# Kernel tuning notes

Hardware: AMD Instinct MI355X
Metric: run time of the kernel (lower is better)

The kernel has to match this reference:

```python
import jax, jax.numpy as jnp
import numpy as np

V = 30000   # vocab (from get_word_embedding default)
D = 640     # d_model
L = 6       # num_layers
H = 8       # num_heads
DH = D // H # head dim 80
FF = 4 * D  # ffn hidden 2560
BOS = 1
EOS = 2
LN_EPS = 1e-6


def _ln(x, s, b):
    m = x.mean(-1, keepdims=True)
    v = ((x - m) ** 2).mean(-1, keepdims=True)
    return (x - m) / jnp.sqrt(v + LN_EPS) * s + b


def _get_logits(tokens, seq_len, emb, Wq, bq, Wk, bk, Wv, bv, Wo, bo,
                ln1s, ln1b, W1, b1, W2, b2, ln2s, ln2b, lmW, lmb):
    # tokens: (B,S) int; seq_len: (B,) int
    B, S = tokens.shape
    h = emb[tokens]                                   # (B,S,D), no pos-enc / scaling in source
    look_ahead = jnp.triu(jnp.ones((S, S), jnp.float32), k=1)          # 1 = masked (TF-style)
    pad = (jnp.arange(S)[None, :] >= seq_len[:, None]).astype(jnp.float32)  # (B,S)
    mask = jnp.maximum(look_ahead[None, None, :, :], pad[:, None, None, :])  # (B,1,S,S)

    def layer(h, p):
        wq, bq_, wk, bk_, wv, bv_, wo, bo_, l1s, l1b, w1, b1_, w2, b2_, l2s, l2b = p
        q = (h @ wq + bq_).reshape(B, S, H, DH)
        k = (h @ wk + bk_).reshape(B, S, H, DH)
        v = (h @ wv + bv_).reshape(B, S, H, DH)
        scores = jnp.einsum('bqhd,bkhd->bhqk', q, k) / jnp.sqrt(jnp.float32(DH))
        scores = scores - mask * 1e9
        a = jax.nn.softmax(scores, axis=-1)
        o = jnp.einsum('bhqk,bkhd->bqhd', a, v).reshape(B, S, D) @ wo + bo_
        h = _ln(h + o, l1s, l1b)                      # post-LN residual
        f = jax.nn.relu(h @ w1 + b1_) @ w2 + b2_
        h = _ln(h + f, l2s, l2b)
        return h, None

    h, _ = jax.lax.scan(layer, h, (Wq, bq, Wk, bk, Wv, bv, Wo, bo,
                                   ln1s, ln1b, W1, b1, W2, b2, ln2s, ln2b))
    return h @ lmW + lmb                              # (B,S,V)


def setup_inputs() -> dict:
    key = jax.random.key(0)
    ks = jax.random.split(key, 12)
    std = 0.02

    def n(k, shape):
        return jax.random.normal(k, shape, jnp.float32) * std

    return {
        'initial_words': jax.random.randint(ks[0], (4, 8), 3, V, dtype=jnp.int32),
        'max_length': 32,
        'emb': n(ks[1], (V, D)),
        'Wq': n(ks[2], (L, D, D)), 'bq': jnp.zeros((L, D), jnp.float32),
        'Wk': n(ks[3], (L, D, D)), 'bk': jnp.zeros((L, D), jnp.float32),
        'Wv': n(ks[4], (L, D, D)), 'bv': jnp.zeros((L, D), jnp.float32),
        'Wo': n(ks[5], (L, D, D)), 'bo': jnp.zeros((L, D), jnp.float32),
        'ln1s': jnp.ones((L, D), jnp.float32), 'ln1b': jnp.zeros((L, D), jnp.float32),
        'W1': n(ks[6], (L, D, FF)), 'b1': jnp.zeros((L, FF), jnp.float32),
        'W2': n(ks[7], (L, FF, D)), 'b2': jnp.zeros((L, D), jnp.float32),
        'ln2s': jnp.ones((L, D), jnp.float32), 'ln2b': jnp.zeros((L, D), jnp.float32),
        'lmW': n(ks[8], (D, V)), 'lmb': jnp.zeros((V,), jnp.float32),
    }


def reference(initial_words, max_length, emb, Wq, bq, Wk, bk, Wv, bv, Wo, bo,
              ln1s, ln1b, W1, b1, W2, b2, ln2s, ln2b, lmW, lmb):
    B, init_len = initial_words.shape
    seq_len = jnp.full((B,), max_length, jnp.int32)
    S = max_length + 1  # BOS + max_length slots, as in the torch padding logic
    inp = (jnp.zeros((B, S), jnp.int32)
           .at[:, 0].set(BOS)
           .at[:, 1:1 + init_len].set(initial_words.astype(jnp.int32)))

    def cond(c):
        _inp, cl, tok = c
        return (cl + 1 <= max_length) & jnp.any(tok != EOS)

    def body(c):
        inp, cl, _tok = c
        logits = _get_logits(inp, seq_len, emb, Wq, bq, Wk, bk, Wv, bv, Wo, bo,
                             ln1s, ln1b, W1, b1, W2, b2, ln2s, ln2b, lmW, lmb)
        step_logits = jax.lax.dynamic_index_in_dim(logits, cl, axis=1, keepdims=False)
        tok = jnp.argmax(step_logits, axis=-1).astype(jnp.int32)
        inp = inp.at[:, cl + 1].set(tok)
        return (inp, cl + 1, tok)

    inp, _, _ = jax.lax.while_loop(
        cond, body,
        (inp, jnp.int32(init_len), jnp.full((B,), -100, jnp.int32)))
    return inp[:, 1:]
```

## Files before the change

kernel.cpp:

```cpp
#include <hip/hip_runtime.h>
#include <math.h>

#define B 4
#define SEQ 33
#define MAXLEN 32
#define D 640
#define NH 8
#define DH 80
#define NL 6
#define FF 2560
#define V 30000
#define INITLEN 8
#define NBLK 1024
#define NT 256
#define EOS_TOK 2
#define NPOS_P 9
#define NR_P 36
#define LM_NB 938

#define QKV_N 120
#define AW_B 120
#define RF_B 184
#define F1_B 188
#define F2_B 348
#define RL_B 428

#define NFLAGS 1024
#define NSLOT 32
#define SLOT_U 16

#define VER(t,l) ((size_t)((t) * NL + (l)))

typedef float f4 __attribute__((ext_vector_type(4)));

struct Par {
  const int* iw;
  const float* emb;
  const float *Wq, *bq, *Wk, *bk, *Wv, *bv, *Wo, *bo;
  const float *ln1s, *ln1b, *W1, *b1, *W2, *b2, *ln2s, *ln2b, *lmW, *lmb;
  int* out;
};

__device__ __align__(256) float g_Kc[(size_t)NL * B * NH * SEQ * DH];
__device__ __align__(256) float g_Vc[(size_t)NL * B * NH * SEQ * DH];
__device__ __align__(256) float g_xv[(size_t)SEQ * NL * 2560];
__device__ __align__(256) float g_h1v[(size_t)SEQ * NL * 2560];
__device__ __align__(256) float g_qv[(size_t)SEQ * NL * 2560];
__device__ __align__(256) float g_opartv[(size_t)SEQ * NL * 20480];
__device__ __align__(256) float g_f1v[(size_t)SEQ * NL * 10240];
__device__ __align__(256) float g_f2v[(size_t)SEQ * NL * 5120];
__device__ __align__(256) float g_xlm[(size_t)SEQ * 2560];
__device__ __align__(256) int   g_tokv[SEQ * 64];
__device__ __align__(256) int   g_stopv[SEQ * 64];
__device__ float g_xp[NR_P * D];
__device__ float g_h1p[NR_P * D];
__device__ float g_qkvpP[(size_t)8 * 1920 * NR_P];
__device__ float g_qP[(size_t)NH * NR_P * DH];
__device__ float g_opartP[(size_t)NH * D * NR_P];
__device__ float g_f1pP[(size_t)8 * FF * NR_P];
__device__ float g_f2pP[(size_t)32 * D * NR_P];
__device__ unsigned long long g_keys[(size_t)NBLK * B];
__device__ int g_tokens[B * SEQ];
__device__ unsigned g_flags[(size_t)NFLAGS * NSLOT * SLOT_U];
__device__ unsigned g_arrive = 0;
__device__ unsigned g_gen = 0;

#define KCIDX(l,b,h,pos,j) (((((size_t)(l)*B+(b))*NH+(h))*SEQ+(pos))*DH+(j))

__device__ __forceinline__ float ldc(const float* p) {
  return __hip_atomic_load(p, __ATOMIC_RELAXED, __HIP_MEMORY_SCOPE_AGENT);
}
__device__ __forceinline__ void stc(float* p, float v) {
  __hip_atomic_store(p, v, __ATOMIC_RELAXED, __HIP_MEMORY_SCOPE_AGENT);
}
__device__ __forceinline__ int ldci(const int* p) {
  return __hip_atomic_load(p, __ATOMIC_RELAXED, __HIP_MEMORY_SCOPE_AGENT);
}
__device__ __forceinline__ void stci(int* p, int v) {
  __hip_atomic_store(p, v, __ATOMIC_RELAXED, __HIP_MEMORY_SCOPE_AGENT);
}
__device__ __forceinline__ void stcu64(unsigned long long* p, unsigned long long v) {
  __hip_atomic_store(p, v, __ATOMIC_RELAXED, __HIP_MEMORY_SCOPE_AGENT);
}
__device__ __forceinline__ void st4c(float* p, f4 v) {
  asm volatile("global_store_dwordx4 %0, %1, off sc1" :: "v"(p), "v"(v) : "memory");
}
__device__ __forceinline__ void ld4c_issue(f4& dst, const float* p) {
  asm volatile("global_load_dwordx4 %0, %1, off sc1" : "=v"(dst) : "v"(p) : "memory");
}
__device__ __forceinline__ void wait_vm() {
  asm volatile("s_waitcnt vmcnt(0)" ::: "memory");
  __builtin_amdgcn_sched_barrier(0);
}
__device__ __forceinline__ unsigned long long mk64(float lo, float hi) {
  return ((unsigned long long)__float_as_uint(hi) << 32) | (unsigned long long)__float_as_uint(lo);
}

__device__ __forceinline__ void gsync_full() {
  __syncthreads();
  if (threadIdx.x == 0) {
    __threadfence();
    unsigned g = __hip_atomic_load(&g_gen, __ATOMIC_SEQ_CST, __HIP_MEMORY_SCOPE_AGENT);
    unsigned old = __hip_atomic_fetch_add(&g_arrive, 1u, __ATOMIC_SEQ_CST, __HIP_MEMORY_SCOPE_AGENT);
    if (old == NBLK - 1u) {
      __hip_atomic_store(&g_arrive, 0u, __ATOMIC_SEQ_CST, __HIP_MEMORY_SCOPE_AGENT);
      __hip_atomic_fetch_add(&g_gen, 1u, __ATOMIC_SEQ_CST, __HIP_MEMORY_SCOPE_AGENT);
    } else {
      while (__hip_atomic_load(&g_gen, __ATOMIC_RELAXED, __HIP_MEMORY_SCOPE_AGENT) == g)
        __builtin_amdgcn_s_sleep(2);
    }
    __threadfence();
  }
  __syncthreads();
}

__device__ __forceinline__ void stage_done(int idx) {
  asm volatile("s_waitcnt vmcnt(0)" ::: "memory");
  __syncthreads();
  if (threadIdx.x == 0) {
    __hip_atomic_fetch_add(
        &g_flags[((size_t)idx * NSLOT + (blockIdx.x & (NSLOT - 1))) * SLOT_U],
        1u, __ATOMIC_RELAXED, __HIP_MEMORY_SCOPE_AGENT);
  }
}

__device__ __forceinline__ void stage_wait(int idx, unsigned cnt) {
  if (threadIdx.x < 64) {
    const unsigned* base = &g_flags[(size_t)idx * NSLOT * SLOT_U];
    int spins = 0;
    for (;;) {
      unsigned v = 0u;
      if (threadIdx.x < NSLOT)
        v = __hip_atomic_load(base + (size_t)threadIdx.x * SLOT_U,
                              __ATOMIC_RELAXED, __HIP_MEMORY_SCOPE_AGENT);
      #pragma unroll
      for (int o = 16; o > 0; o >>= 1) v += __shfl_down(v, o, 64);
      v = __shfl(v, 0, 64);
      if (v >= cnt) break;
      if (spins < 16)      __builtin_amdgcn_s_sleep(1);
      else if (spins < 96) __builtin_amdgcn_s_sleep(16);
      else                 __builtin_amdgcn_s_sleep(127);
      ++spins;
    }
  }
  __syncthreads();
  asm volatile("" ::: "memory");
}

__device__ __forceinline__ float bred_sum(float v, float* s_red) {
  #pragma unroll
  for (int o = 32; o > 0; o >>= 1) v += __shfl_down(v, o, 64);
  __syncthreads();
  if ((threadIdx.x & 63) == 0) s_red[threadIdx.x >> 6] = v;
  __syncthreads();
  return s_red[0] + s_red[1] + s_red[2] + s_red[3];
}

__device__ void ln_inplace(float* row, const float* gam, const float* bet, float* s_red) {
  float ps = 0.f;
  for (int d = threadIdx.x; d < D; d += NT) ps += row[d];
  const float m = bred_sum(ps, s_red) * (1.0f / 640.0f);
  float pv = 0.f;
  for (int d = threadIdx.x; d < D; d += NT) { float t = row[d] - m; pv += t * t; }
  const float var = bred_sum(pv, s_red) * (1.0f / 640.0f);
  const float rstd = 1.0f / sqrtf(var + 1e-6f);
  for (int d = threadIdx.x; d < D; d += NT)
    row[d] = (row[d] - m) * rstd * gam[d] + bet[d];
  __syncthreads();
}


__device__ void st_QKV(const Par& p, int l, int t, float* s_x, float* s_t, float* s_r) {
  const int tid = threadIdx.x;
  const int cg = (blockIdx.x & 7) * 15 + (blockIdx.x >> 3);
  const int m = cg / 40, colm0 = (cg % 40) * 16;
  const int w = tid >> 6, lane = tid & 63;
  if (l == 0) {
    const int tok = g_tokv[t * 64 + w];
    for (int c4 = lane; c4 < 160; c4 += 64)
      *(f4*)&s_x[w * 640 + c4 * 4] = *(const f4*)&p.emb[(size_t)tok * D + c4 * 4];
  } else {
    const size_t ver = VER(t, l - 1);
    const float* h1 = g_h1v + ver * 2560 + w * 640;
    const float* fa = g_f2v + ver * 5120 + w * 640;
    const float* fb = g_f2v + ver * 5120 + 2560 + w * 640;
    const float* b2 = p.b2 + (size_t)(l - 1) * D;
    for (int c4 = lane; c4 < 160; c4 += 64) {
      f4 a = *(const f4*)&h1[c4 * 4];
      f4 b = *(const f4*)&fa[c4 * 4];
      f4 c = *(const f4*)&fb[c4 * 4];
      const float* bb = b2 + c4 * 4;
      f4 s = { a.x + b.x + c.x + bb[0], a.y + b.y + c.y + bb[1],
               a.z + b.z + c.z + bb[2], a.w + b.w + c.w + bb[3] };
      *(f4*)&s_x[w * 640 + c4 * 4] = s;
    }
    float ps = 0.f;
    for (int i = lane; i < D; i += 64) ps += s_x[w * 640 + i];
    #pragma unroll
    for (int o = 32; o > 0; o >>= 1) ps += __shfl_xor(ps, o, 64);
    const float mean = ps * (1.0f / 640.0f);
    float pv = 0.f;
    for (int i = lane; i < D; i += 64) { float d = s_x[w * 640 + i] - mean; pv += d * d; }
    #pragma unroll
    for (int o = 32; o > 0; o >>= 1) pv += __shfl_xor(pv, o, 64);
    const float rstd = 1.0f / sqrtf(pv * (1.0f / 640.0f) + 1e-6f);
    const float* gam = p.ln2s + (size_t)(l - 1) * D;
    const float* bet = p.ln2b + (size_t)(l - 1) * D;
    for (int i = lane; i < D; i += 64)
      s_x[w * 640 + i] = (s_x[w * 640 + i] - mean) * rstd * gam[i] + bet[i];
  }
  __syncthreads();
  if (cg == 0) {
    const size_t xo = VER(t, l) * 2560;
    for (int i = tid; i < 640; i += NT)
      st4c(&g_xv[xo + (size_t)i * 4], *(f4*)&s_x[i * 4]);
  }
  const int ds = tid >> 4, c = tid & 15;
  const float* Wb = (m == 0 ? p.Wq : m == 1 ? p.Wk : p.Wv)
                    + (size_t)l * D * D + colm0 + c;
  float a0 = 0, a1 = 0, a2 = 0, a3 = 0;
  #pragma unroll
  for (int kb = 0; kb < 40; kb += 20) {
    float wv[20];
    #pragma unroll
    for (int j = 0; j < 20; ++j) wv[j] = Wb[(size_t)(ds + (kb + j) * 16) * D];
    #pragma unroll
    for (int j = 0; j < 20; ++j) {
      const int dd = ds + (kb + j) * 16;
      a0 = fmaf(s_x[dd],        wv[j], a0);
      a1 = fmaf(s_x[640 + dd],  wv[j], a1);
      a2 = fmaf(s_x[1280 + dd], wv[j], a2);
      a3 = fmaf(s_x[1920 + dd], wv[j], a3);
    }
  }
  { f4 av = { a0, a1, a2, a3 }; *(f4*)&s_t[c * 68 + ds * 4] = av; }
  __syncthreads();
  if (tid < 64) {
    const int c2 = tid >> 2, b = tid & 3;
    float v = 0.f;
    #pragma unroll
    for (int d2 = 0; d2 < 16; ++d2) v += s_t[c2 * 68 + d2 * 4 + b];
    v += (m == 0 ? p.bq : m == 1 ? p.bk : p.bv)[(size_t)l * D + colm0 + c2];
    s_r[c2 * 4 + b] = v;
  }
  __syncthreads();
  if (m == 0) {
    if (tid < 16) {
      f4 v = { s_r[tid * 4], s_r[tid * 4 + 1], s_r[tid * 4 + 2], s_r[tid * 4 + 3] };
      st4c(&g_qv[VER(t, l) * 2560 + (size_t)(colm0 + tid) * 4], v);
    }
  } else {
    const int h = colm0 / 80, j0 = colm0 % 80;
    if (tid < 16) {
      const int cq = tid & 3, b = tid >> 2;
      f4 v = { s_r[(cq*4+0)*4+b], s_r[(cq*4+1)*4+b], s_r[(cq*4+2)*4+b], s_r[(cq*4+3)*4+b] };
      float* cache = (m == 1) ? g_Kc : g_Vc;
      st4c(&cache[KCIDX(l, b, h, t, j0 + cq * 4)], v);
    }
  }
}

__device__ void st_AW(const Par& p, int l, int t,
                      float* s_q, float* s_sc, float* s_o, float* s_wo) {
  const int idx = blockIdx.x - AW_B, h = idx >> 3, c = idx & 7, tid = threadIdx.x;
  const size_t qo = VER(t, l) * 2560;
  if (tid < 80) {
    f4 q = *(const f4*)&g_qv[qo + (size_t)(h * 80 + tid) * 4];
    s_q[tid] = q.x; s_q[80 + tid] = q.y; s_q[160 + tid] = q.z; s_q[240 + tid] = q.w;
  }
  __syncthreads();
  const int nk = t + 1;
  for (int task = tid; task < 4 * nk; task += NT) {
    const int b = task / nk, kp = task % nk;
    const float* qq = s_q + b * 80;
    const f4* kk = (const f4*)&g_Kc[KCIDX(l, b, h, kp, 0)];
    float sd = 0.f;
    #pragma unroll
    for (int j4 = 0; j4 < 20; ++j4) {
      f4 k4 = kk[j4];
      sd += qq[j4*4+0]*k4.x + qq[j4*4+1]*k4.y + qq[j4*4+2]*k4.z + qq[j4*4+3]*k4.w;
    }
    s_sc[b * 33 + kp] = sd / 8.94427190999915878564f;
  }
  __syncthreads();
  if (tid < 4) {
    const int b = tid;
    float m = -1e30f;
    for (int k = 0; k < nk; ++k) m = fmaxf(m, s_sc[b * 33 + k]);
    float sum = 0.f;
    for (int k = 0; k < nk; ++k) { float e = expf(s_sc[b * 33 + k] - m); s_sc[b * 33 + k] = e; sum += e; }
    s_sc[132 + b] = 1.0f / sum;
  }
  __syncthreads();
  if (tid < 80) {
    const int b = tid / 20, j4 = tid % 20;
    f4 acc = { 0.f, 0.f, 0.f, 0.f };
    for (int kp = 0; kp < nk; ++kp) {
      f4 v = *(const f4*)&g_Vc[KCIDX(l, b, h, kp, j4 * 4)];
      const float wgt = s_sc[b * 33 + kp];
      acc.x += wgt * v.x; acc.y += wgt * v.y; acc.z += wgt * v.z; acc.w += wgt * v.w;
    }
    const float r = s_sc[132 + b];
    f4 o = { acc.x * r, acc.y * r, acc.z * r, acc.w * r };
    *(f4*)&s_o[b * 80 + j4 * 4] = o;
  }
  __syncthreads();
  if (tid < 240) {
    const int j = tid % 80, sub = tid / 80;
    const int col = c * 80 + j;
    const int d0 = sub * 27, d1 = (sub == 2) ? 80 : d0 + 27;
    const float* Wo = p.Wo + (size_t)l * D * D + col;
    float a0 = 0, a1 = 0, a2 = 0, a3 = 0;
    #pragma unroll 9
    for (int dd = d0; dd < d1; ++dd) {
      const float w = Wo[(size_t)(h * 80 + dd) * D];
      a0 += s_o[0*80+dd] * w; a1 += s_o[80+dd] * w;
      a2 += s_o[160+dd] * w; a3 += s_o[240+dd] * w;
    }
    float* tp = s_wo + (j * 3 + sub) * 4;
    tp[0] = a0; tp[1] = a1; tp[2] = a2; tp[3] = a3;
  }
  __syncthreads();
  if (tid < 80) {
    const int b = tid / 20, cq = tid % 20;
    f4 v;
    #pragma unroll
    for (int i = 0; i < 4; ++i) {
      const int j = cq * 4 + i;
      v[i] = s_wo[(j*3+0)*4+b] + s_wo[(j*3+1)*4+b] + s_wo[(j*3+2)*4+b];
    }
    st4c(&g_opartv[VER(t, l) * 20480 + (size_t)(h * 4 + b) * 640 + c * 80 + cq * 4], v);
  }
}

__device__ void st_RF(const Par& p, int l, int t, float* s_row, float* s_red) {
  const int b = blockIdx.x - RF_B, tid = threadIdx.x;
  const size_t ver = VER(t, l);
  if (tid < 160) {
    f4 xv = *(const f4*)&g_xv[ver * 2560 + (size_t)b * 640 + tid * 4];
    const float* bo = p.bo + (size_t)l * D + tid * 4;
    f4 a;
    a.x = xv.x + bo[0]; a.y = xv.y + bo[1]; a.z = xv.z + bo[2]; a.w = xv.w + bo[3];
    #pragma unroll
    for (int h = 0; h < 8; ++h) {
      f4 ov = *(const f4*)&g_opartv[ver * 20480 + (size_t)(h * 4 + b) * 640 + tid * 4];
      a.x += ov.x; a.y += ov.y; a.z += ov.z; a.w += ov.w;
    }
    *(f4*)&s_row[tid * 4] = a;
  }
  __syncthreads();
  ln_inplace(s_row, p.ln1s + (size_t)l * D, p.ln1b + (size_t)l * D, s_red);
  if (tid < 160) st4c(&g_h1v[ver * 2560 + (size_t)b * 640 + tid * 4], *(f4*)&s_row[tid * 4]);
}

__device__ void st_F1(const Par& p, int l, int t, float* s_x, float* s_t, float* s_r) {
  const int tid = threadIdx.x;
  const int raw = blockIdx.x - F1_B;
  const int cg = (raw & 7) * 20 + (raw >> 3);
  const int col0 = cg * 16;
  const size_t ver = VER(t, l);
  #pragma unroll
  for (int i = 0; i < 3; ++i) {
    const int idx = tid + i * NT;
    if (idx < 640) *(f4*)&s_x[idx * 4] = *(const f4*)&g_h1v[ver * 2560 + (size_t)idx * 4];
  }
  __syncthreads();
  const int ds = tid >> 4, c = tid & 15;
  const float* Wb = p.W1 + (size_t)l * D * FF + col0 + c;
  float a0 = 0, a1 = 0, a2 = 0, a3 = 0;
  #pragma unroll
  for (int kb = 0; kb < 40; kb += 20) {
    float wv[20];
    #pragma unroll
    for (int j = 0; j < 20; ++j) wv[j] = Wb[(size_t)(ds + (kb + j) * 16) * FF];
    #pragma unroll
    for (int j = 0; j < 20; ++j) {
      const int dd = ds + (kb + j) * 16;
      a0 = fmaf(s_x[dd],        wv[j], a0);
      a1 = fmaf(s_x[640 + dd],  wv[j], a1);
      a2 = fmaf(s_x[1280 + dd], wv[j], a2);
      a3 = fmaf(s_x[1920 + dd], wv[j], a3);
    }
  }
  { f4 av = { a0, a1, a2, a3 }; *(f4*)&s_t[c * 68 + ds * 4] = av; }
  __syncthreads();
  if (tid < 64) {
    const int c2 = tid >> 2, b = tid & 3;
    float v = 0.f;
    #pragma unroll
    for (int d2 = 0; d2 < 16; ++d2) v += s_t[c2 * 68 + d2 * 4 + b];
    v += p.b1[(size_t)l * FF + col0 + c2];
    s_r[c2 * 4 + b] = fmaxf(v, 0.f);
  }
  __syncthreads();
  if (tid < 16) {
    const int cq = tid & 3, b = tid >> 2;
    f4 v = { s_r[(cq*4+0)*4+b], s_r[(cq*4+1)*4+b], s_r[(cq*4+2)*4+b], s_r[(cq*4+3)*4+b] };
    st4c(&g_f1v[ver * 10240 + (size_t)b * 2560 + col0 + cq * 4], v);
  }
}

__device__ void st_F2(const Par& p, int l, int t, float* s_f, float* s_t, float* s_r) {
  const int idx = blockIdx.x - F2_B, tid = threadIdx.x;
  const int hf = idx / 40, craw = idx % 40;
  const int cg = (craw & 7) * 5 + (craw >> 3);
  const int col0 = cg * 16;
  const size_t ver = VER(t, l);
  #pragma unroll
  for (int i = 0; i < 5; ++i) {
    const int ii = tid + i * NT;
    const int b = ii / 320, fo = ii % 320;
    *(f4*)&s_f[b * 1280 + fo * 4] =
        *(const f4*)&g_f1v[ver * 10240 + (size_t)b * 2560 + hf * 1280 + fo * 4];
  }
  __syncthreads();
  const int ds = tid >> 4, c = tid & 15;
  const float* Wb = p.W2 + (size_t)l * FF * D + (size_t)hf * 1280 * D + col0 + c;
  float a0 = 0, a1 = 0, a2 = 0, a3 = 0;
  #pragma unroll
  for (int kb = 0; kb < 80; kb += 20) {
    float wv[20];
    #pragma unroll
    for (int j = 0; j < 20; ++j) wv[j] = Wb[(size_t)(ds + (kb + j) * 16) * D];
    #pragma unroll
    for (int j = 0; j < 20; ++j) {
      const int dl = ds + (kb + j) * 16;
      a0 = fmaf(s_f[dl],        wv[j], a0);
      a1 = fmaf(s_f[1280 + dl], wv[j], a1);
      a2 = fmaf(s_f[2560 + dl], wv[j], a2);
      a3 = fmaf(s_f[3840 + dl], wv[j], a3);
    }
  }
  { f4 av = { a0, a1, a2, a3 }; *(f4*)&s_t[c * 68 + ds * 4] = av; }
  __syncthreads();
  if (tid < 64) {
    const int c2 = tid >> 2, b = tid & 3;
    float v = 0.f;
    #pragma unroll
    for (int d2 = 0; d2 < 16; ++d2) v += s_t[c2 * 68 + d2 * 4 + b];
    s_r[c2 * 4 + b] = v;
  }
  __syncthreads();
  if (tid < 16) {
    const int cq = tid & 3, b = tid >> 2;
    f4 v = { s_r[(cq*4+0)*4+b], s_r[(cq*4+1)*4+b], s_r[(cq*4+2)*4+b], s_r[(cq*4+3)*4+b] };
    st4c(&g_f2v[ver * 5120 + (size_t)(hf * 4 + b) * 640 + col0 + cq * 4], v);
  }
}

__device__ void st_RL(const Par& p, int t, float* s_row, float* s_red) {
  const int b = blockIdx.x - RL_B, tid = threadIdx.x;
  const size_t ver = VER(t, NL - 1);
  if (tid < 160) {
    f4 h  = *(const f4*)&g_h1v[ver * 2560 + (size_t)b * 640 + tid * 4];
    f4 fa = *(const f4*)&g_f2v[ver * 5120 + (size_t)b * 640 + tid * 4];
    f4 fb = *(const f4*)&g_f2v[ver * 5120 + 2560 + (size_t)b * 640 + tid * 4];
    const float* b2 = p.b2 + (size_t)(NL - 1) * D + tid * 4;
    f4 a;
    a.x = h.x + fa.x + fb.x + b2[0];
    a.y = h.y + fa.y + fb.y + b2[1];
    a.z = h.z + fa.z + fb.z + b2[2];
    a.w = h.w + fa.w + fb.w + b2[3];
    *(f4*)&s_row[tid * 4] = a;
  }
  __syncthreads();
  ln_inplace(s_row, p.ln2s + (size_t)(NL - 1) * D, p.ln2b + (size_t)(NL - 1) * D, s_red);
  if (tid < 160)
    st4c(&g_xlm[(size_t)t * 2560 + (size_t)b * 640 + tid * 4], *(f4*)&s_row[tid * 4]);
}

__device__ void st_LM(const Par& p, int t, float* s_xf, float* s_part, unsigned long long* s_key) {
  const int bid = blockIdx.x, tid = threadIdx.x;
  const int xcd = bid & 7, jj = bid >> 3;
  const int chunk = (xcd < 2 ? xcd * 118 : 236 + (xcd - 2) * 117) + jj;
  #pragma unroll
  for (int i = 0; i < 3; ++i) {
    const int idx = tid + i * NT;
    if (idx < 640) *(f4*)&s_xf[idx * 4] = *(const f4*)&g_xlm[(size_t)t * 2560 + (size_t)idx * 4];
  }
  __syncthreads();
  const int sg = tid >> 5, cj = tid & 31;
  const int col = chunk * 32 + cj;
  float a0 = 0, a1 = 0, a2 = 0, a3 = 0;
  if (col < V) {
    const float* W = p.lmW + (size_t)sg * 80 * V + col;
    #pragma unroll
    for (int kb = 0; kb < 80; kb += 20) {
      float w[20];
      #pragma unroll
      for (int j = 0; j < 20; ++j) w[j] = W[(size_t)(kb + j) * V];
      #pragma unroll
      for (int j = 0; j < 20; ++j) {
        const int d = sg * 80 + kb + j;
        a0 = fmaf(s_xf[d],        w[j], a0);
        a1 = fmaf(s_xf[640 + d],  w[j], a1);
        a2 = fmaf(s_xf[1280 + d], w[j], a2);
        a3 = fmaf(s_xf[1920 + d], w[j], a3);
      }
    }
  }
  float* tp = s_part + (sg * 32 + cj) * 4;
  tp[0] = a0; tp[1] = a1; tp[2] = a2; tp[3] = a3;
  __syncthreads();
  if (tid < 128) {
    const int cj2 = tid >> 2, b = tid & 3, col2 = chunk * 32 + cj2;
    unsigned long long key = 0ull;
    if (col2 < V) {
      float a = p.lmb[col2];
      #pragma unroll
      for (int sg2 = 0; sg2 < 8; ++sg2) a += s_part[(sg2 * 32 + cj2) * 4 + b];
      unsigned u = __float_as_uint(a);
      u = (u & 0x80000000u) ? ~u : (u | 0x80000000u);
      key = ((unsigned long long)u << 32) | (unsigned)(V - col2);
    }
    s_key[cj2 * 4 + b] = key;
  }
  __syncthreads();
  if (tid < 4) {
    unsigned long long k0 = 0ull;
    for (int cj2 = 0; cj2 < 32; ++cj2) {
      const unsigned long long k = s_key[cj2 * 4 + tid];
      if (k > k0) k0 = k;
    }
    stcu64(&g_keys[(size_t)bid * B + tid], k0);
  }
}

__device__ void st_CTL(int t, unsigned long long* s_k64, int* s_ctl) {
  const int tid = threadIdx.x;
  const int i0 = tid, i1 = tid + NT, i2 = tid + 2 * NT, i3 = tid + 3 * NT;
  f4 z = { 0.f, 0.f, 0.f, 0.f };
  f4 ka0, kb0, ka1, kb1, ka2, kb2, ka3 = z, kb3 = z;
  ld4c_issue(ka0, (const float*)&g_keys[(size_t)i0 * 4]);
  ld4c_issue(kb0, (const float*)&g_keys[(size_t)i0 * 4 + 2]);
  ld4c_issue(ka1, (const float*)&g_keys[(size_t)i1 * 4]);
  ld4c_issue(kb1, (const float*)&g_keys[(size_t)i1 * 4 + 2]);
  ld4c_issue(ka2, (const float*)&g_keys[(size_t)i2 * 4]);
  ld4c_issue(kb2, (const float*)&g_keys[(size_t)i2 * 4 + 2]);
  if (i3 < LM_NB) {
    ld4c_issue(ka3, (const float*)&g_keys[(size_t)i3 * 4]);
    ld4c_issue(kb3, (const float*)&g_keys[(size_t)i3 * 4 + 2]);
  }
  wait_vm();
  unsigned long long m0 = mk64(ka0.x, ka0.y), m1 = mk64(ka0.z, ka0.w);
  unsigned long long m2 = mk64(kb0.x, kb0.y), m3 = mk64(kb0.z, kb0.w);
  { unsigned long long s;
    s = mk64(ka1.x,ka1.y); if (s>m0) m0=s;  s = mk64(ka1.z,ka1.w); if (s>m1) m1=s;
    s = mk64(kb1.x,kb1.y); if (s>m2) m2=s;  s = mk64(kb1.z,kb1.w); if (s>m3) m3=s;
    s = mk64(ka2.x,ka2.y); if (s>m0) m0=s;  s = mk64(ka2.z,ka2.w); if (s>m1) m1=s;
    s = mk64(kb2.x,kb2.y); if (s>m2) m2=s;  s = mk64(kb2.z,kb2.w); if (s>m3) m3=s;
    s = mk64(ka3.x,ka3.y); if (s>m0) m0=s;  s = mk64(ka3.z,ka3.w); if (s>m1) m1=s;
    s = mk64(kb3.x,kb3.y); if (s>m2) m2=s;  s = mk64(kb3.z,kb3.w); if (s>m3) m3=s;
  }
  #pragma unroll
  for (int o = 32; o > 0; o >>= 1) {
    unsigned long long s;
    s = __shfl_down(m0, o, 64); if (s > m0) m0 = s;
    s = __shfl_down(m1, o, 64); if (s > m1) m1 = s;
    s = __shfl_down(m2, o, 64); if (s > m2) m2 = s;
    s = __shfl_down(m3, o, 64); if (s > m3) m3 = s;
  }
  if ((tid & 63) == 0) {
    const int w = tid >> 6;
    s_k64[w * 4 + 0] = m0; s_k64[w * 4 + 1] = m1;
    s_k64[w * 4 + 2] = m2; s_k64[w * 4 + 3] = m3;
  }
  __syncthreads();
  if (tid == 0) {
    #pragma unroll
    for (int b = 0; b < B; ++b) {
      unsigned long long k0 = s_k64[b];
      #pragma unroll
      for (int w = 1; w < 4; ++w) if (s_k64[w * 4 + b] > k0) k0 = s_k64[w * 4 + b];
      const int tok = V - (int)(unsigned)(k0 & 0xFFFFFFFFull);
      stci(&g_tokens[b * SEQ + t + 1], tok);
      stci(&g_tokv[(t + 1) * 64 + b], tok);
      s_ctl[b] = tok;
    }
    int stop = (t == MAXLEN - 1) ? 1 : 0;
    if (s_ctl[0] == EOS_TOK && s_ctl[1] == EOS_TOK &&
        s_ctl[2] == EOS_TOK && s_ctl[3] == EOS_TOK) stop = 1;
    stci(&g_stopv[t * 64], stop);
  }
}


__device__ void st_Qp(const Par& p, int l, float* s_a) {
  const int idx = blockIdx.x, tid = threadIdx.x;
  const int h = idx / 24, rem = idx % 24, s = rem / 3, rg = rem % 3;
  const int r0 = rg * 12, d0 = s * 80;
  for (int i = tid; i < 960; i += NT) {
    const int ri = i / 80, dd = i % 80;
    s_a[i] = ldc(&g_xp[(r0 + ri) * D + d0 + dd]);
  }
  __syncthreads();
  if (tid < 240) {
    const int m = tid / 80, j = tid % 80, col = h * 80 + j;
    const float* W = (m == 0 ? p.Wq : m == 1 ? p.Wk : p.Wv) + (size_t)l * D * D + col;
    float acc[12];
    #pragma unroll
    for (int ri = 0; ri < 12; ++ri) acc[ri] = 0.f;
    for (int dd = 0; dd < 80; ++dd) {
      const float w = W[(size_t)(d0 + dd) * D];
      #pragma unroll
      for (int ri = 0; ri < 12; ++ri) acc[ri] += s_a[ri * 80 + dd] * w;
    }
    float* o = g_qkvpP + ((size_t)s * 1920 + m * 640 + col) * NR_P + r0;
    #pragma unroll
    for (int ri = 0; ri < 12; ++ri) stc(o + ri, acc[ri]);
  }
}

__device__ void st_AWp1(const Par& p, int l) {
  const int idx = blockIdx.x - 192, h = idx >> 2, c = idx & 3, tid = threadIdx.x;
  for (int pp = c; pp < NPOS_P; pp += 4) {
    for (int task = tid; task < 960; task += NT) {
      const int m = task / 320, rem = task % 320, j = rem >> 2, b = rem & 3;
      const int r = pp * 4 + b;
      const int col = m * 640 + h * 80 + j;
      const float* q = g_qkvpP + (size_t)col * NR_P + r;
      float a = 0.f;
      #pragma unroll
      for (int s = 0; s < 8; ++s) a += ldc(q + (size_t)s * 1920 * NR_P);
      a += (m == 0 ? p.bq : m == 1 ? p.bk : p.bv)[(size_t)l * D + h * 80 + j];
      if (m == 0)      stc(&g_qP[((size_t)h * NR_P + r) * DH + j], a);
      else if (m == 1) stc(&g_Kc[KCIDX(l, b, h, pp, j)], a);
      else             stc(&g_Vc[KCIDX(l, b, h, pp, j)], a);
    }
  }
}

__device__ void st_AWp2(const Par& p, int l, float* s_a, float* s_b, float* s_c) {
  const int idx = blockIdx.x - 224, h = idx >> 2, rg = idx & 3, tid = threadIdx.x;
  const int r0 = rg * 9;
  for (int i = tid; i < 720; i += NT) {
    const int ri = i / 80, j = i % 80;
    s_a[i] = ldc(&g_qP[((size_t)h * NR_P + r0 + ri) * DH + j]);
  }
  __syncthreads();
  for (int task = tid; task < 81; task += NT) {
    const int ri = task / 9, kp = task % 9;
    const int r = r0 + ri, pos = r >> 2, b = r & 3;
    if (kp <= pos) {
      const float* kk = g_Kc + KCIDX(l, b, h, kp, 0);
      const float* qq = s_a + ri * 80;
      float sd = 0.f;
      for (int j = 0; j < 80; ++j) sd += qq[j] * ldc(kk + j);
      s_c[ri * 9 + kp] = sd / 8.94427190999915878564f;
    }
  }
  __syncthreads();
  if (tid < 9) {
    const int ri = tid, r = r0 + ri, pos = r >> 2;
    float m = -1e30f;
    for (int k = 0; k <= pos; ++k) m = fmaxf(m, s_c[ri * 9 + k]);
    float sum = 0.f;
    for (int k = 0; k <= pos; ++k) { float e = expf(s_c[ri * 9 + k] - m); s_c[ri * 9 + k] = e; sum += e; }
    s_c[81 + ri] = 1.0f / sum;
  }
  __syncthreads();
  for (int task = tid; task < 720; task += NT) {
    const int ri = task / 80, j = task % 80;
    const int r = r0 + ri, pos = r >> 2, b = r & 3;
    float acc = 0.f;
    for (int kp = 0; kp <= pos; ++kp)
      acc += s_c[ri * 9 + kp] * ldc(&g_Vc[KCIDX(l, b, h, kp, j)]);
    s_b[ri * 80 + j] = acc * s_c[81 + ri];
  }
  __syncthreads();
  if (tid < 160) {
    for (int pass = 0; pass < 4; ++pass) {
      const int col = pass * 160 + tid;
      const float* Wo = p.Wo + (size_t)l * D * D + col;
      float acc[9];
      #pragma unroll
      for (int ri = 0; ri < 9; ++ri) acc[ri] = 0.f;
      for (int dd = 0; dd < 80; ++dd) {
        const float w = Wo[(size_t)(h * 80 + dd) * D];
        #pragma unroll
        for (int ri = 0; ri < 9; ++ri) acc[ri] += s_b[ri * 80 + dd] * w;
      }
      #pragma unroll
      for (int ri = 0; ri < 9; ++ri)
        stc(&g_opartP[((size_t)h * D + col) * NR_P + r0 + ri], acc[ri]);
    }
  }
}

__device__ void st_RFp(const Par& p, int l, float* s_row, float* s_red) {
  const int r = blockIdx.x, tid = threadIdx.x;
  for (int col = tid; col < D; col += NT) {
    float a = ldc(&g_xp[r * D + col]) + p.bo[(size_t)l * D + col];
    #pragma unroll
    for (int h = 0; h < 8; ++h) a += ldc(&g_opartP[((size_t)h * D + col) * NR_P + r]);
    s_row[col] = a;
  }
  __syncthreads();
  ln_inplace(s_row, p.ln1s + (size_t)l * D, p.ln1b + (size_t)l * D, s_red);
  for (int col = tid; col < D; col += NT) stc(&g_h1p[r * D + col], s_row[col]);
}

__device__ void st_F1p(const Par& p, int l, float* s_a) {
  const int idx = blockIdx.x, tid = threadIdx.x;
  const int s = idx / 30, rem = idx % 30, cg = rem / 3, rg = rem % 3;
  const int r0 = rg * 12, d0 = s * 80;
  for (int i = tid; i < 960; i += NT) {
    const int ri = i / 80, dd = i % 80;
    s_a[i] = ldc(&g_h1p[(r0 + ri) * D + d0 + dd]);
  }
  __syncthreads();
  const int col = cg * 256 + tid;
  const float* W = p.W1 + (size_t)l * D * FF + col;
  float acc[12];
  #pragma unroll
  for (int ri = 0; ri < 12; ++ri) acc[ri] = 0.f;
  for (int dd = 0; dd < 80; ++dd) {
    const float w = W[(size_t)(d0 + dd) * FF];
    #pragma unroll
    for (int ri = 0; ri < 12; ++ri) acc[ri] += s_a[ri * 80 + dd] * w;
  }
  float* o = g_f1pP + ((size_t)s * FF + col) * NR_P + r0;
  #pragma unroll
  for (int ri = 0; ri < 12; ++ri) stc(o + ri, acc[ri]);
}

__device__ void st_F2p(const Par& p, int l, float* s_c) {
  const int idx = blockIdx.x - 240, c = idx / 3, rg = idx % 3, tid = threadIdx.x;
  const int r0 = rg * 12;
  for (int task = tid; task < 960; task += NT) {
    const int ri = task / 80, fj = task % 80;
    const int fcol = c * 80 + fj;
    const float* pp = g_f1pP + (size_t)fcol * NR_P + r0 + ri;
    float a = 0.f;
    #pragma unroll
    for (int s = 0; s < 8; ++s) a += ldc(pp + (size_t)s * FF * NR_P);
    a += p.b1[(size_t)l * FF + fcol];
    s_c[ri * 80 + fj] = fmaxf(a, 0.f);
  }
  __syncthreads();
  for (int pass = 0; pass < 3; ++pass) {
    const int col = pass * 256 + tid;
    if (col < D) {
      const float* W = p.W2 + (size_t)l * FF * D + col;
      float acc[12];
      #pragma unroll
      for (int ri = 0; ri < 12; ++ri) acc[ri] = 0.f;
      for (int fj = 0; fj < 80; ++fj) {
        const float w = W[(size_t)(c * 80 + fj) * D];
        #pragma unroll
        for (int ri = 0; ri < 12; ++ri) acc[ri] += s_c[ri * 80 + fj] * w;
      }
      float* o = g_f2pP + ((size_t)c * D + col) * NR_P + r0;
      #pragma unroll
      for (int ri = 0; ri < 12; ++ri) stc(o + ri, acc[ri]);
    }
  }
}

__device__ void st_RQp(const Par& p, int l, float* s_row, float* s_red) {
  const int r = blockIdx.x, tid = threadIdx.x;
  for (int col = tid; col < D; col += NT) {
    float a = ldc(&g_h1p[r * D + col]) + p.b2[(size_t)l * D + col];
    #pragma unroll 8
    for (int c = 0; c < 32; ++c) a += ldc(&g_f2pP[((size_t)c * D + col) * NR_P + r]);
    s_row[col] = a;
  }
  __syncthreads();
  ln_inplace(s_row, p.ln2s + (size_t)l * D, p.ln2b + (size_t)l * D, s_red);
  for (int col = tid; col < D; col += NT) stc(&g_xp[r * D + col], s_row[col]);
}

__device__ void st_RLp(const Par& p, float* s_row, float* s_red) {
  const int b = blockIdx.x, r = 32 + b, tid = threadIdx.x;
  for (int col = tid; col < D; col += NT) {
    float a = ldc(&g_h1p[r * D + col]) + p.b2[(size_t)(NL - 1) * D + col];
    #pragma unroll 8
    for (int c = 0; c < 32; ++c) a += ldc(&g_f2pP[((size_t)c * D + col) * NR_P + r]);
    s_row[col] = a;
  }
  __syncthreads();
  ln_inplace(s_row, p.ln2s + (size_t)(NL - 1) * D, p.ln2b + (size_t)(NL - 1) * D, s_red);
  for (int col = tid; col < D; col += NT)
    stc(&g_xlm[(size_t)INITLEN * 2560 + (size_t)b * 640 + col], s_row[col]);
}

__global__ __launch_bounds__(NT, 4) void tfgen(Par p) {
  __shared__ float s_pool[6400];
  __shared__ float s_red[8];
  __shared__ unsigned long long s_key[128];
  __shared__ int s_ctl[8];

  const int bid = blockIdx.x, tid = threadIdx.x;
  int ep = 0;

  {
    unsigned* f = g_flags + (size_t)bid * NSLOT * SLOT_U;
    for (int i = tid; i < NSLOT * SLOT_U; i += NT) f[i] = 0u;
  }
  if (bid < NR_P) {
    const int pos = bid >> 2, b = bid & 3;
    const int tk = (pos == 0) ? 1 : p.iw[b * INITLEN + pos - 1];
    for (int d = tid; d < D; d += NT) stc(&g_xp[bid * D + d], p.emb[(size_t)tk * D + d]);
  }
  if (bid == NBLK - 1) {
    for (int i = tid; i < B * SEQ; i += NT) {
      const int b = i / SEQ, pos = i % SEQ;
      int tk = 0;
      if (pos == 0) tk = 1;
      else if (pos <= INITLEN) tk = p.iw[b * INITLEN + pos - 1];
      stci(&g_tokens[i], tk);
    }
  }
  gsync_full();

  float* ps_x  = s_pool;
  float* ps_a  = s_pool + 2560;
  float* ps_b  = s_pool + 3584;
  float* ps_c  = s_pool + 4352;
  int eRQ = -1, eF2last = -1;
  for (int l = 0; l < NL; ++l) {
    const int eQ = ep++;
    if (bid < 192) { if (l > 0) stage_wait(eRQ, 36); st_Qp(p, l, ps_a); stage_done(eQ); }
    const int eA1 = ep++;
    if (bid >= 192 && bid < 224) { stage_wait(eQ, 192); st_AWp1(p, l); stage_done(eA1); }
    const int eA2 = ep++;
    if (bid >= 224 && bid < 256) { stage_wait(eA1, 32); st_AWp2(p, l, ps_a, ps_b, ps_c); stage_done(eA2); }
    const int eRF = ep++;
    if (bid < NR_P) { stage_wait(eA2, 32); st_RFp(p, l, ps_x, s_red); stage_done(eRF); }
    const int eF1 = ep++;
    if (bid < 240) { stage_wait(eRF, 36); st_F1p(p, l, ps_a); stage_done(eF1); }
    const int eF2 = ep++;
    if (bid >= 240 && bid < 336) { stage_wait(eF1, 240); st_F2p(p, l, ps_c); stage_done(eF2); }
    eF2last = eF2;
    if (l < NL - 1) {
      eRQ = ep++;
      if (bid < NR_P) { stage_wait(eF2, 96); st_RQp(p, l, ps_x, s_red); stage_done(eRQ); }
    }
  }

  for (int t = INITLEN;; ++t) {
    int eCTL;
    if (t == INITLEN) {
      const int eRLp = ep++;
      if (bid < 4) { stage_wait(eF2last, 96); st_RLp(p, s_pool, s_red); stage_done(eRLp); }
      const int eLM = ep++;
      if (bid < LM_NB) { stage_wait(eRLp, 4); st_LM(p, t, s_pool, s_pool + 2560, s_key); stage_done(eLM); }
      eCTL = ep++;
      if (bid == NBLK - 1) { stage_wait(eLM, LM_NB); st_CTL(t, s_key, s_ctl); stage_done(eCTL); }
    } else {
      int eF2s = -1;
      for (int l = 0; l < NL; ++l) {
        const int eQKV = ep++;
        if (bid < QKV_N) {
          if (l > 0) stage_wait(eF2s, 80);
          st_QKV(p, l, t, s_pool, s_pool + 2560, s_pool + 3648);
          stage_done(eQKV);
        }
        const int eAW = ep++;
        if (bid >= AW_B && bid < RF_B) {
          stage_wait(eQKV, QKV_N);
          st_AW(p, l, t, s_pool, s_pool + 320, s_pool + 480, s_pool + 800);
          stage_done(eAW);
        }
        const int eRF = ep++;
        if (bid >= RF_B && bid < F1_B) { stage_wait(eAW, 64); st_RF(p, l, t, s_pool, s_red); stage_done(eRF); }
        const int eF1 = ep++;
        if (bid >= F1_B && bid < F2_B) {
          stage_wait(eRF, 4);
          st_F1(p, l, t, s_pool, s_pool + 2560, s_pool + 3648);
          stage_done(eF1);
        }
        eF2s = ep++;
        if (bid >= F2_B && bid < RL_B) {
          stage_wait(eF1, 160);
          st_F2(p, l, t, s_pool, s_pool + 5120, s_pool + 6208);
          stage_done(eF2s);
        }
      }
      const int eRL = ep++;
      if (bid >= RL_B && bid < RL_B + 4) { stage_wait(eF2s, 80); st_RL(p, t, s_pool, s_red); stage_done(eRL); }
      const int eLM = ep++;
      if (bid < LM_NB) { stage_wait(eRL, 4); st_LM(p, t, s_pool, s_pool + 2560, s_key); stage_done(eLM); }
      eCTL = ep++;
      if (bid == NBLK - 1) { stage_wait(eLM, LM_NB); st_CTL(t, s_key, s_ctl); stage_done(eCTL); }
    }
    stage_wait(eCTL, 1);
    if (g_stopv[t * 64]) break;
  }

  if (bid == 0) {
    for (int i = tid; i < B * MAXLEN; i += NT) {
      const int b = i >> 5, j = i & 31;
      p.out[i] = ldci(&g_tokens[b * SEQ + j + 1]);
    }
  }
}

extern "C" void kernel_launch(void* const* d_in, const int* in_sizes, int n_in,
                              void* d_out, int out_size, void* d_ws, size_t ws_size,
                              hipStream_t stream)
{
  (void)in_sizes; (void)n_in; (void)out_size; (void)d_ws; (void)ws_size;
  Par p;
  p.iw   = (const int*)  d_in[0];
  p.emb  = (const float*)d_in[2];
  p.Wq   = (const float*)d_in[3];  p.bq   = (const float*)d_in[4];
  p.Wk   = (const float*)d_in[5];  p.bk   = (const float*)d_in[6];
  p.Wv   = (const float*)d_in[7];  p.bv   = (const float*)d_in[8];
  p.Wo   = (const float*)d_in[9];  p.bo   = (const float*)d_in[10];
  p.ln1s = (const float*)d_in[11]; p.ln1b = (const float*)d_in[12];
  p.W1   = (const float*)d_in[13]; p.b1   = (const float*)d_in[14];
  p.W2   = (const float*)d_in[15]; p.b2   = (const float*)d_in[16];
  p.ln2s = (const float*)d_in[17]; p.ln2b = (const float*)d_in[18];
  p.lmW  = (const float*)d_in[19]; p.lmb  = (const float*)d_in[20];
  p.out  = (int*)d_out;

  void* args[] = { (void*)&p };
  hipError_t err = hipLaunchCooperativeKernel((const void*)tfgen, dim3(NBLK), dim3(NT),
                                              args, 0, stream);
  if (err != hipSuccess) {
    hipLaunchKernelGGL(tfgen, dim3(NBLK), dim3(NT), 0, stream, p);
  }
}
```

Before: 17.39 ms.

## Fuse residual+LayerNorm stages into consumers to remove grid-wide barrier stages

```diff
diff --git a/kernel.cpp b/kernel.cpp
--- a/kernel.cpp
+++ b/kernel.cpp
@@ -20,10 +20,10 @@
 
 #define QKV_N 120
 #define AW_B 120
-#define RF_B 184
+#define AW_E 184
 #define F1_B 188
 #define F2_B 348
-#define RL_B 428
+#define F2_E 428
 
 #define NFLAGS 1024
 #define NSLOT 32
@@ -137,9 +137,9 @@
       for (int o = 16; o > 0; o >>= 1) v += __shfl_down(v, o, 64);
       v = __shfl(v, 0, 64);
       if (v >= cnt) break;
-      if (spins < 16)      __builtin_amdgcn_s_sleep(1);
-      else if (spins < 96) __builtin_amdgcn_s_sleep(16);
-      else                 __builtin_amdgcn_s_sleep(127);
+      if (spins < 16)       __builtin_amdgcn_s_sleep(1);
+      else if (spins < 128) __builtin_amdgcn_s_sleep(8);
+      else                  __builtin_amdgcn_s_sleep(32);
       ++spins;
     }
   }
@@ -169,6 +169,41 @@
   __syncthreads();
 }
 
+__device__ __forceinline__ void ln_wave(float* s_x, const float* gam, const float* bet) {
+  const int tid = threadIdx.x, w = tid >> 6, lane = tid & 63;
+  float ps = 0.f;
+  for (int i = lane; i < D; i += 64) ps += s_x[w * 640 + i];
+  #pragma unroll
+  for (int o = 32; o > 0; o >>= 1) ps += __shfl_xor(ps, o, 64);
+  const float mean = ps * (1.0f / 640.0f);
+  float pv = 0.f;
+  for (int i = lane; i < D; i += 64) { float d = s_x[w * 640 + i] - mean; pv += d * d; }
+  #pragma unroll
+  for (int o = 32; o > 0; o >>= 1) pv += __shfl_xor(pv, o, 64);
+  const float rstd = 1.0f / sqrtf(pv * (1.0f / 640.0f) + 1e-6f);
+  for (int i = lane; i < D; i += 64)
+    s_x[w * 640 + i] = (s_x[w * 640 + i] - mean) * rstd * gam[i] + bet[i];
+}
+
+__device__ __forceinline__ void build_x2w(const Par& p, int t, int lsrc, float* s_x) {
+  const int tid = threadIdx.x, w = tid >> 6, lane = tid & 63;
+  const size_t ver = VER(t, lsrc);
+  const float* h1 = g_h1v + ver * 2560 + w * 640;
+  const float* fa = g_f2v + ver * 5120 + w * 640;
+  const float* fb = g_f2v + ver * 5120 + 2560 + w * 640;
+  const float* b2 = p.b2 + (size_t)lsrc * D;
+  for (int c4 = lane; c4 < 160; c4 += 64) {
+    f4 a = *(const f4*)&h1[c4 * 4];
+    f4 b = *(const f4*)&fa[c4 * 4];
+    f4 c = *(const f4*)&fb[c4 * 4];
+    const float* bb = b2 + c4 * 4;
+    f4 s = { a.x + b.x + c.x + bb[0], a.y + b.y + c.y + bb[1],
+             a.z + b.z + c.z + bb[2], a.w + b.w + c.w + bb[3] };
+    *(f4*)&s_x[w * 640 + c4 * 4] = s;
+  }
+  ln_wave(s_x, p.ln2s + (size_t)lsrc * D, p.ln2b + (size_t)lsrc * D);
+}
+
 
 __device__ void st_QKV(const Par& p, int l, int t, float* s_x, float* s_t, float* s_r) {
   const int tid = threadIdx.x;
@@ -180,34 +215,7 @@
     for (int c4 = lane; c4 < 160; c4 += 64)
       *(f4*)&s_x[w * 640 + c4 * 4] = *(const f4*)&p.emb[(size_t)tok * D + c4 * 4];
   } else {
-    const size_t ver = VER(t, l - 1);
-    const float* h1 = g_h1v + ver * 2560 + w * 640;
-    const float* fa = g_f2v + ver * 5120 + w * 640;
-    const float* fb = g_f2v + ver * 5120 + 2560 + w * 640;
-    const float* b2 = p.b2 + (size_t)(l - 1) * D;
-    for (int c4 = lane; c4 < 160; c4 += 64) {
-      f4 a = *(const f4*)&h1[c4 * 4];
-      f4 b = *(const f4*)&fa[c4 * 4];
-      f4 c = *(const f4*)&fb[c4 * 4];
-      const float* bb = b2 + c4 * 4;
-      f4 s = { a.x + b.x + c.x + bb[0], a.y + b.y + c.y + bb[1],
-               a.z + b.z + c.z + bb[2], a.w + b.w + c.w + bb[3] };
-      *(f4*)&s_x[w * 640 + c4 * 4] = s;
-    }
-    float ps = 0.f;
-    for (int i = lane; i < D; i += 64) ps += s_x[w * 640 + i];
-    #pragma unroll
-    for (int o = 32; o > 0; o >>= 1) ps += __shfl_xor(ps, o, 64);
-    const float mean = ps * (1.0f / 640.0f);
-    float pv = 0.f;
-    for (int i = lane; i < D; i += 64) { float d = s_x[w * 640 + i] - mean; pv += d * d; }
-    #pragma unroll
-    for (int o = 32; o > 0; o >>= 1) pv += __shfl_xor(pv, o, 64);
-    const float rstd = 1.0f / sqrtf(pv * (1.0f / 640.0f) + 1e-6f);
-    const float* gam = p.ln2s + (size_t)(l - 1) * D;
-    const float* bet = p.ln2b + (size_t)(l - 1) * D;
-    for (int i = lane; i < D; i += 64)
-      s_x[w * 640 + i] = (s_x[w * 640 + i] - mean) * rstd * gam[i] + bet[i];
+    build_x2w(p, t, l - 1, s_x);
   }
   __syncthreads();
   if (cg == 0) {
@@ -333,38 +341,34 @@
   }
 }
 
-__device__ void st_RF(const Par& p, int l, int t, float* s_row, float* s_red) {
-  const int b = blockIdx.x - RF_B, tid = threadIdx.x;
-  const size_t ver = VER(t, l);
-  if (tid < 160) {
-    f4 xv = *(const f4*)&g_xv[ver * 2560 + (size_t)b * 640 + tid * 4];
-    const float* bo = p.bo + (size_t)l * D + tid * 4;
-    f4 a;
-    a.x = xv.x + bo[0]; a.y = xv.y + bo[1]; a.z = xv.z + bo[2]; a.w = xv.w + bo[3];
-    #pragma unroll
-    for (int h = 0; h < 8; ++h) {
-      f4 ov = *(const f4*)&g_opartv[ver * 20480 + (size_t)(h * 4 + b) * 640 + tid * 4];
-      a.x += ov.x; a.y += ov.y; a.z += ov.z; a.w += ov.w;
-    }
-    *(f4*)&s_row[tid * 4] = a;
-  }
-  __syncthreads();
-  ln_inplace(s_row, p.ln1s + (size_t)l * D, p.ln1b + (size_t)l * D, s_red);
-  if (tid < 160) st4c(&g_h1v[ver * 2560 + (size_t)b * 640 + tid * 4], *(f4*)&s_row[tid * 4]);
-}
-
 __device__ void st_F1(const Par& p, int l, int t, float* s_x, float* s_t, float* s_r) {
   const int tid = threadIdx.x;
   const int raw = blockIdx.x - F1_B;
   const int cg = (raw & 7) * 20 + (raw >> 3);
   const int col0 = cg * 16;
   const size_t ver = VER(t, l);
-  #pragma unroll
-  for (int i = 0; i < 3; ++i) {
-    const int idx = tid + i * NT;
-    if (idx < 640) *(f4*)&s_x[idx * 4] = *(const f4*)&g_h1v[ver * 2560 + (size_t)idx * 4];
-  }
-  __syncthreads();
+  const int w = tid >> 6, lane = tid & 63;
+  {
+    const float* xv = g_xv + ver * 2560 + w * 640;
+    const float* bo = p.bo + (size_t)l * D;
+    for (int c4 = lane; c4 < 160; c4 += 64) {
+      f4 a = *(const f4*)&xv[c4 * 4];
+      const float* bb = bo + c4 * 4;
+      a.x += bb[0]; a.y += bb[1]; a.z += bb[2]; a.w += bb[3];
+      #pragma unroll
+      for (int h = 0; h < 8; ++h) {
+        f4 ov = *(const f4*)&g_opartv[ver * 20480 + (size_t)(h * 4 + w) * 640 + c4 * 4];
+        a.x += ov.x; a.y += ov.y; a.z += ov.z; a.w += ov.w;
+      }
+      *(f4*)&s_x[w * 640 + c4 * 4] = a;
+    }
+    ln_wave(s_x, p.ln1s + (size_t)l * D, p.ln1b + (size_t)l * D);
+  }
+  __syncthreads();
+  if (cg == 0) {
+    for (int i = tid; i < 640; i += NT)
+      st4c(&g_h1v[ver * 2560 + (size_t)i * 4], *(f4*)&s_x[i * 4]);
+  }
   const int ds = tid >> 4, c = tid & 15;
   const float* Wb = p.W1 + (size_t)l * D * FF + col0 + c;
   float a0 = 0, a1 = 0, a2 = 0, a3 = 0;
@@ -448,35 +452,19 @@
   }
 }
 
-__device__ void st_RL(const Par& p, int t, float* s_row, float* s_red) {
-  const int b = blockIdx.x - RL_B, tid = threadIdx.x;
-  const size_t ver = VER(t, NL - 1);
-  if (tid < 160) {
-    f4 h  = *(const f4*)&g_h1v[ver * 2560 + (size_t)b * 640 + tid * 4];
-    f4 fa = *(const f4*)&g_f2v[ver * 5120 + (size_t)b * 640 + tid * 4];
-    f4 fb = *(const f4*)&g_f2v[ver * 5120 + 2560 + (size_t)b * 640 + tid * 4];
-    const float* b2 = p.b2 + (size_t)(NL - 1) * D + tid * 4;
-    f4 a;
-    a.x = h.x + fa.x + fb.x + b2[0];
-    a.y = h.y + fa.y + fb.y + b2[1];
-    a.z = h.z + fa.z + fb.z + b2[2];
-    a.w = h.w + fa.w + fb.w + b2[3];
-    *(f4*)&s_row[tid * 4] = a;
-  }
-  __syncthreads();
-  ln_inplace(s_row, p.ln2s + (size_t)(NL - 1) * D, p.ln2b + (size_t)(NL - 1) * D, s_red);
-  if (tid < 160)
-    st4c(&g_xlm[(size_t)t * 2560 + (size_t)b * 640 + tid * 4], *(f4*)&s_row[tid * 4]);
-}
-
-__device__ void st_LM(const Par& p, int t, float* s_xf, float* s_part, unsigned long long* s_key) {
+__device__ void st_LM(const Par& p, int t, int src, float* s_xf, float* s_part,
+                      unsigned long long* s_key) {
   const int bid = blockIdx.x, tid = threadIdx.x;
   const int xcd = bid & 7, jj = bid >> 3;
   const int chunk = (xcd < 2 ? xcd * 118 : 236 + (xcd - 2) * 117) + jj;
-  #pragma unroll
-  for (int i = 0; i < 3; ++i) {
-    const int idx = tid + i * NT;
-    if (idx < 640) *(f4*)&s_xf[idx * 4] = *(const f4*)&g_xlm[(size_t)t * 2560 + (size_t)idx * 4];
+  if (src == 0) {
+    #pragma unroll
+    for (int i = 0; i < 3; ++i) {
+      const int idx = tid + i * NT;
+      if (idx < 640) *(f4*)&s_xf[idx * 4] = *(const f4*)&g_xlm[(size_t)t * 2560 + (size_t)idx * 4];
+    }
+  } else {
+    build_x2w(p, t, NL - 1, s_xf);
   }
   __syncthreads();
   const int sg = tid >> 5, cj = tid & 31;
@@ -844,7 +832,7 @@
       const int eRLp = ep++;
       if (bid < 4) { stage_wait(eF2last, 96); st_RLp(p, s_pool, s_red); stage_done(eRLp); }
       const int eLM = ep++;
-      if (bid < LM_NB) { stage_wait(eRLp, 4); st_LM(p, t, s_pool, s_pool + 2560, s_key); stage_done(eLM); }
+      if (bid < LM_NB) { stage_wait(eRLp, 4); st_LM(p, t, 0, s_pool, s_pool + 2560, s_key); stage_done(eLM); }
       eCTL = ep++;
       if (bid == NBLK - 1) { stage_wait(eLM, LM_NB); st_CTL(t, s_key, s_ctl); stage_done(eCTL); }
     } else {
@@ -857,30 +845,26 @@
           stage_done(eQKV);
         }
         const int eAW = ep++;
-        if (bid >= AW_B && bid < RF_B) {
+        if (bid >= AW_B && bid < AW_E) {
           stage_wait(eQKV, QKV_N);
           st_AW(p, l, t, s_pool, s_pool + 320, s_pool + 480, s_pool + 800);
           stage_done(eAW);
         }
-        const int eRF = ep++;
-        if (bid >= RF_B && bid < F1_B) { stage_wait(eAW, 64); st_RF(p, l, t, s_pool, s_red); stage_done(eRF); }
         const int eF1 = ep++;
         if (bid >= F1_B && bid < F2_B) {
-          stage_wait(eRF, 4);
+          stage_wait(eAW, 64);
           st_F1(p, l, t, s_pool, s_pool + 2560, s_pool + 3648);
           stage_done(eF1);
         }
         eF2s = ep++;
-        if (bid >= F2_B && bid < RL_B) {
+        if (bid >= F2_B && bid < F2_E) {
           stage_wait(eF1, 160);
           st_F2(p, l, t, s_pool, s_pool + 5120, s_pool + 6208);
           stage_done(eF2s);
         }
       }
-      const int eRL = ep++;
-      if (bid >= RL_B && bid < RL_B + 4) { stage_wait(eF2s, 80); st_RL(p, t, s_pool, s_red); stage_done(eRL); }
       const int eLM = ep++;
-      if (bid < LM_NB) { stage_wait(eRL, 4); st_LM(p, t, s_pool, s_pool + 2560, s_key); stage_done(eLM); }
+      if (bid < LM_NB) { stage_wait(eF2s, 80); st_LM(p, t, 1, s_pool, s_pool + 2560, s_key); stage_done(eLM); }
       eCTL = ep++;
       if (bid == NBLK - 1) { stage_wait(eLM, LM_NB); st_CTL(t, s_key, s_ctl); stage_done(eCTL); }
     }
```

After: 16.34 ms. -6.1%, faster.
